# Optimization experiments

Measured on AMD Instinct MI355X. Metric: run time of the kernel, lower is better.

Reference implementation:

```python
import jax, jax.numpy as jnp
import numpy as np

B, S, D_MODEL, D_OUT = 4, 4096, 512, 64


def setup_inputs() -> dict:
    key = jax.random.key(0)
    ks = jax.random.split(key, 10)
    query = jax.random.normal(ks[0], (B, S, D_MODEL), dtype=jnp.float32)
    key_t = jax.random.normal(ks[1], (B, S, D_MODEL), dtype=jnp.float32)
    value = jax.random.normal(ks[2], (B, S, D_MODEL), dtype=jnp.float32)
    mask = jax.random.randint(ks[3], (B, S, S), 0, 2, dtype=jnp.int32)
    sc = 1.0 / np.sqrt(D_MODEL)
    Wq = jax.random.uniform(ks[4], (D_MODEL, D_OUT), minval=-sc, maxval=sc, dtype=jnp.float32)
    bq = jnp.zeros((D_OUT,), dtype=jnp.float32)
    Wk = jax.random.uniform(ks[5], (D_MODEL, D_OUT), minval=-sc, maxval=sc, dtype=jnp.float32)
    bk = jnp.zeros((D_OUT,), dtype=jnp.float32)
    Wv = jax.random.uniform(ks[6], (D_MODEL, D_OUT), minval=-sc, maxval=sc, dtype=jnp.float32)
    bv = jnp.zeros((D_OUT,), dtype=jnp.float32)
    return {"query": query, "key": key_t, "value": value, "mask": mask,
            "Wq": Wq, "bq": bq, "Wk": Wk, "bk": bk, "Wv": Wv, "bv": bv}


def reference(query, key, value, mask, Wq, bq, Wk, bk, Wv, bv):
    # Linear projections (single head): [B,S,D_MODEL] @ [D_MODEL,D_OUT] + bias
    q = jnp.einsum('bsd,de->bse', query, Wq) + bq
    k = jnp.einsum('bsd,de->bse', key, Wk) + bk
    v = jnp.einsum('bsd,de->bse', value, Wv) + bv
    dim_k = k.shape[-1]
    scores = jnp.einsum('bqe,bke->bqk', q, k) / jnp.sqrt(jnp.float32(dim_k))  # [B,S,S]
    scores = jnp.where(mask == 0, -jnp.inf, scores)
    weights = jax.nn.softmax(scores, axis=-1)
    # dropout is identity in eval mode / for deterministic reference
    outputs = jnp.einsum('bqk,bke->bqe', weights, v)  # [B,S,D_OUT]
    return outputs
```

## Files before the change

### kernel.cpp

```cpp
#include <hip/hip_runtime.h>
#include <hip/hip_bf16.h>

#define BB 4
#define SS 4096
#define DMODEL 512
#define DOUT 64
#define NKH 2
#define KH (SS / NKH)
#define NIT (KH / 64)

typedef __bf16 bf16_t;
typedef __bf16 bf16x8 __attribute__((ext_vector_type(8)));
typedef float floatx4 __attribute__((ext_vector_type(4)));

__device__ inline void gl_lds16(const void* g, void* l) {
  __builtin_amdgcn_global_load_lds(
      (const __attribute__((address_space(1))) unsigned int*)g,
      (__attribute__((address_space(3))) unsigned int*)l, 16, 0, 0);
}

__global__ __launch_bounds__(256) void wtrans_kernel(
    const float* __restrict__ Wq, const float* __restrict__ Wk,
    const float* __restrict__ Wv, bf16_t* __restrict__ wT) {
  int idx = blockIdx.x * 256 + threadIdx.x;
  int mat = idx >> 12;
  int r   = idx & 4095;
  int e   = r & 63;
  int d0  = (r >> 6) << 3;
  const float* W = (mat == 0) ? Wq : ((mat == 1) ? Wk : Wv);
  bf16_t* dst = wT + (size_t)mat * (DOUT * DMODEL) + (size_t)e * DMODEL + d0;
#pragma unroll
  for (int j = 0; j < 8; ++j) dst[j] = (bf16_t)W[(size_t)(d0 + j) * DOUT + e];
}

__global__ __launch_bounds__(256) void proj_kernel(
    const float* __restrict__ inq, const float* __restrict__ ink,
    const float* __restrict__ inv, const bf16_t* __restrict__ wT,
    const float* __restrict__ bq, const float* __restrict__ bk,
    const float* __restrict__ bv,
    bf16_t* __restrict__ q_ws, bf16_t* __restrict__ k_ws,
    bf16_t* __restrict__ v_wsT) {
  const int mat = blockIdx.x >> 8;
  const int s0  = (blockIdx.x & 255) << 6;
  const int lane = threadIdx.x & 63;
  const int w    = threadIdx.x >> 6;
  const int col  = lane & 15, quad = lane >> 4;

  const float* inp  = (mat == 0) ? inq : ((mat == 1) ? ink : inv);
  const float* bias = (mat == 0) ? bq : ((mat == 1) ? bk : bv);
  const bf16_t* wt  = wT + (size_t)mat * (DOUT * DMODEL);

  const int arow = s0 + w * 16 + col;
  floatx4 acc[4] = {};

  for (int ch = 0; ch < 16; ++ch) {
    const int d0 = ch * 32 + quad * 8;
    float4 a0 = *(const float4*)(inp + (size_t)arow * DMODEL + d0);
    float4 a1 = *(const float4*)(inp + (size_t)arow * DMODEL + d0 + 4);
    bf16x8 af;
    af[0] = (bf16_t)a0.x; af[1] = (bf16_t)a0.y; af[2] = (bf16_t)a0.z; af[3] = (bf16_t)a0.w;
    af[4] = (bf16_t)a1.x; af[5] = (bf16_t)a1.y; af[6] = (bf16_t)a1.z; af[7] = (bf16_t)a1.w;
#pragma unroll
    for (int c = 0; c < 4; ++c) {
      bf16x8 bw = *(const bf16x8*)(wt + (size_t)(c * 16 + col) * DMODEL + d0);
      acc[c] = __builtin_amdgcn_mfma_f32_16x16x32_bf16(af, bw, acc[c], 0, 0, 0);
    }
  }

#pragma unroll
  for (int c = 0; c < 4; ++c) {
    float bcol = bias[c * 16 + col];
#pragma unroll
    for (int r = 0; r < 4; ++r) {
      int row = s0 + w * 16 + quad * 4 + r;
      float v = acc[c][r] + bcol;
      if (mat == 2) {
        int b = row >> 12, sp = row & 4095;
        v_wsT[((size_t)(b * DOUT + c * 16 + col)) * SS + sp] = (bf16_t)v;
      } else {
        bf16_t* dst = (mat == 0) ? q_ws : k_ws;
        dst[(size_t)row * DOUT + c * 16 + col] = (bf16_t)v;
      }
    }
  }
}

__global__ __launch_bounds__(256, 2) void attn_kernel(
    const bf16_t* __restrict__ q_ws, const bf16_t* __restrict__ k_ws,
    const bf16_t* __restrict__ v_wsT, const int* __restrict__ mask,
    float* __restrict__ O_part, float* __restrict__ l_part) {
  const int bq = blockIdx.x >> 1, kh = blockIdx.x & 1;
  const int b  = bq >> 6;
  const int q0 = (bq & 63) << 6;
  const int kbase = kh * KH;
  const int lane = threadIdx.x & 63;
  const int wi   = threadIdx.x >> 6;
  const int col  = lane & 15, quad = lane >> 4;

  __shared__ __align__(16) bf16_t Kb[2][64 * 64];
  __shared__ __align__(16) bf16_t Vb[2][64 * 64];
  __shared__ __align__(16) bf16_t Pl[4][16][72];

  const int qrowA = q0 + wi * 16 + col;
  const bf16_t* qbase = q_ws + ((size_t)(b * SS) + qrowA) * DOUT + quad * 8;
  const bf16x8 qa0 = *(const bf16x8*)(qbase);
  const bf16x8 qa1 = *(const bf16x8*)(qbase + 32);
  const int* mrow = mask + ((size_t)(b * SS) + qrowA) * SS + quad * 8;

  const int srow = lane >> 3;
  const int schk = (lane & 7) ^ srow;

  auto stage = [&](int it, int buf) {
    const int k0 = kbase + it * 64;
#pragma unroll
    for (int j = 0; j < 2; ++j) {
      const int i = wi * 2 + j;
      const int r = i * 8 + srow;
      const char* gK = (const char*)(k_ws + ((size_t)(b * SS) + k0 + r) * DOUT) + schk * 16;
      gl_lds16(gK, (char*)(&Kb[buf][0]) + i * 1024);
      const char* gV = (const char*)(v_wsT + ((size_t)(b * DOUT) + r) * SS + k0) + schk * 16;
      gl_lds16(gV, (char*)(&Vb[buf][0]) + i * 1024);
    }
  };

  int4 mc[2][2], mn[2][2];
  auto loadM = [&](int k0, int4 m[2][2]) {
#pragma unroll
    for (int s = 0; s < 2; ++s) {
      const int4* mp = (const int4*)(mrow + k0 + s * 32);
      m[s][0] = mp[0];
      m[s][1] = mp[1];
    }
  };

  floatx4 o[4] = {};
  float l_acc = 0.f;
  const bf16_t* prow_r = &Pl[wi][col][quad * 8];

  stage(0, 0);
  loadM(kbase, mc);
  __syncthreads();

  for (int it = 0; it < NIT; ++it) {
    const int buf = it & 1;
    const int itn = (it + 1 < NIT) ? it + 1 : it;

    loadM(kbase + itn * 64, mn);
    stage(itn, buf ^ 1);

    floatx4 sacc[4];
#pragma unroll
    for (int c = 0; c < 4; ++c) {
      const int row = c * 16 + col;
      bf16x8 k0f = *(const bf16x8*)((const char*)&Kb[buf][0] + row * 128 + ((quad ^ (col & 7)) * 16));
      bf16x8 k1f = *(const bf16x8*)((const char*)&Kb[buf][0] + row * 128 + (((4 | quad) ^ (col & 7)) * 16));
      floatx4 z = {};
      z = __builtin_amdgcn_mfma_f32_16x16x32_bf16(qa0, k0f, z, 0, 0, 0);
      z = __builtin_amdgcn_mfma_f32_16x16x32_bf16(qa1, k1f, z, 0, 0, 0);
      sacc[c] = z;
    }

    bf16x8 vc[4][2];
#pragma unroll
    for (int c = 0; c < 4; ++c) {
      const int row = c * 16 + col;
      vc[c][0] = *(const bf16x8*)((const char*)&Vb[buf][0] + row * 128 + ((quad ^ (col & 7)) * 16));
      vc[c][1] = *(const bf16x8*)((const char*)&Vb[buf][0] + row * 128 + (((4 | quad) ^ (col & 7)) * 16));
    }

#pragma unroll
    for (int c = 0; c < 4; ++c)
#pragma unroll
      for (int r = 0; r < 4; ++r)
        Pl[wi][quad * 4 + r][c * 16 + col] = (bf16_t)__expf(sacc[c][r] * 0.125f);

    asm volatile("s_waitcnt lgkmcnt(0)" ::: "memory");

    bf16x8 pa0 = *(const bf16x8*)(prow_r);
    bf16x8 pa1 = *(const bf16x8*)(prow_r + 32);

    float lp = 0.f;
    bf16x8 pm0, pm1;
    auto apply = [&](bf16x8 pa, int4 mlo, int4 mhi, bf16x8& pm) {
      int mm[8] = {mlo.x, mlo.y, mlo.z, mlo.w, mhi.x, mhi.y, mhi.z, mhi.w};
#pragma unroll
      for (int j = 0; j < 8; ++j) {
        bf16_t pv = (mm[j] != 0) ? pa[j] : (bf16_t)0.0f;
        pm[j] = pv;
        lp += (float)pv;
      }
    };
    apply(pa0, mc[0][0], mc[0][1], pm0);
    apply(pa1, mc[1][0], mc[1][1], pm1);
    lp += __shfl_xor(lp, 16);
    lp += __shfl_xor(lp, 32);
    l_acc += lp;

#pragma unroll
    for (int c = 0; c < 4; ++c) {
      o[c] = __builtin_amdgcn_mfma_f32_16x16x32_bf16(pm0, vc[c][0], o[c], 0, 0, 0);
      o[c] = __builtin_amdgcn_mfma_f32_16x16x32_bf16(pm1, vc[c][1], o[c], 0, 0, 0);
    }

    mc[0][0] = mn[0][0]; mc[0][1] = mn[0][1];
    mc[1][0] = mn[1][0]; mc[1][1] = mn[1][1];

    __syncthreads();
  }

  float* Op = O_part + (size_t)blockIdx.x * 64 * 64;
#pragma unroll
  for (int c = 0; c < 4; ++c)
#pragma unroll
    for (int r = 0; r < 4; ++r)
      Op[(wi * 16 + quad * 4 + r) * 64 + c * 16 + col] = o[c][r];
  if (quad == 0) l_part[(size_t)blockIdx.x * 64 + wi * 16 + col] = l_acc;
}

__global__ __launch_bounds__(256) void combine_kernel(
    const float* __restrict__ O_part, const float* __restrict__ l_part,
    float* __restrict__ out) {
  const int idx = blockIdx.x * 256 + threadIdx.x;
  const int base = idx * 4;
  const int row = base >> 6;
  const int c   = base & 63;
  const int t   = row >> 6;
  const int rl  = row & 63;
  const float* p0 = O_part + (((size_t)(t * 2 + 0) * 64 + rl) * 64 + c);
  const float* p1 = O_part + (((size_t)(t * 2 + 1) * 64 + rl) * 64 + c);
  const float inv = 1.0f / (l_part[(size_t)(t * 2) * 64 + rl] +
                            l_part[(size_t)(t * 2 + 1) * 64 + rl]);
  float4 a = *(const float4*)p0;
  float4 b = *(const float4*)p1;
  float4 r4 = {(a.x + b.x) * inv, (a.y + b.y) * inv,
               (a.z + b.z) * inv, (a.w + b.w) * inv};
  *(float4*)(out + base) = r4;
}

extern "C" void kernel_launch(void* const* d_in, const int* in_sizes, int n_in,
                              void* d_out, int out_size, void* d_ws, size_t ws_size,
                              hipStream_t stream) {
  const float* query = (const float*)d_in[0];
  const float* key   = (const float*)d_in[1];
  const float* value = (const float*)d_in[2];
  const int*   mask  = (const int*)d_in[3];
  const float* Wq = (const float*)d_in[4];
  const float* bq = (const float*)d_in[5];
  const float* Wk = (const float*)d_in[6];
  const float* bk = (const float*)d_in[7];
  const float* Wv = (const float*)d_in[8];
  const float* bv = (const float*)d_in[9];
  float* out = (float*)d_out;

  bf16_t* q_ws  = (bf16_t*)d_ws;
  bf16_t* k_ws  = q_ws + (size_t)BB * SS * DOUT;
  bf16_t* v_wsT = k_ws + (size_t)BB * SS * DOUT;
  bf16_t* wT    = v_wsT + (size_t)BB * SS * DOUT;
  float*  O_part = (float*)(wT + 3 * DOUT * DMODEL);
  float*  l_part = O_part + (size_t)512 * 64 * 64;

  hipLaunchKernelGGL(wtrans_kernel, dim3(48), dim3(256), 0, stream, Wq, Wk, Wv, wT);
  hipLaunchKernelGGL(proj_kernel, dim3(768), dim3(256), 0, stream,
                     query, key, value, wT, bq, bk, bv, q_ws, k_ws, v_wsT);
  hipLaunchKernelGGL(attn_kernel, dim3(512), dim3(256), 0, stream,
                     q_ws, k_ws, v_wsT, mask, O_part, l_part);
  hipLaunchKernelGGL(combine_kernel, dim3(1024), dim3(256), 0, stream,
                     O_part, l_part, out);
}
```

Measured before the change: 473.6 us.

## Pre-pack int32 attention mask into bitmask with a separate ballot kernel

Adds a maskpack kernel that streams the int32 mask once and uses wave ballots to compress it into 64-bit bitmasks, one bit per key. The attention kernel then loads one u64 per row per 64-key tile instead of 256 bytes of int32 mask, and selects probabilities with bit tests. The goal is to take the large, latency-heavy mask stream out of the attention inner loop and shrink register pressure there. In exchange it adds an extra kernel launch that still reads the full mask, so total mask traffic is not reduced.

```diff
diff --git a/kernel.cpp b/kernel.cpp
--- a/kernel.cpp
+++ b/kernel.cpp
@@ -12,6 +12,8 @@
 typedef __bf16 bf16_t;
 typedef __bf16 bf16x8 __attribute__((ext_vector_type(8)));
 typedef float floatx4 __attribute__((ext_vector_type(4)));
+typedef unsigned long long u64;
+typedef u64 u64x2 __attribute__((ext_vector_type(2)));
 
 __device__ inline void gl_lds16(const void* g, void* l) {
   __builtin_amdgcn_global_load_lds(
@@ -31,6 +33,25 @@
   bf16_t* dst = wT + (size_t)mat * (DOUT * DMODEL) + (size_t)e * DMODEL + d0;
 #pragma unroll
   for (int j = 0; j < 8; ++j) dst[j] = (bf16_t)W[(size_t)(d0 + j) * DOUT + e];
+}
+
+__global__ __launch_bounds__(256) void maskpack_kernel(
+    const int* __restrict__ mask, u64* __restrict__ bits) {
+  const int wid  = (blockIdx.x * 256 + threadIdx.x) >> 6;
+  const int lane = threadIdx.x & 63;
+  const int* base = mask + (size_t)wid * 1024;
+  u64* wbase = bits + (size_t)wid * 16;
+#pragma unroll
+  for (int c = 0; c < 4; ++c) {
+    const int* p = base + c * 256;
+    u64 b0 = __ballot(p[lane] != 0);
+    u64 b1 = __ballot(p[lane + 64] != 0);
+    u64 b2 = __ballot(p[lane + 128] != 0);
+    u64 b3 = __ballot(p[lane + 192] != 0);
+    u64x2 w01 = {b0, b1}, w23 = {b2, b3};
+    if (lane == 0) *(u64x2*)(wbase + c * 4) = w01;
+    if (lane == 1) *(u64x2*)(wbase + c * 4 + 2) = w23;
+  }
 }
 
 __global__ __launch_bounds__(256) void proj_kernel(
@@ -87,7 +108,7 @@
 
 __global__ __launch_bounds__(256, 2) void attn_kernel(
     const bf16_t* __restrict__ q_ws, const bf16_t* __restrict__ k_ws,
-    const bf16_t* __restrict__ v_wsT, const int* __restrict__ mask,
+    const bf16_t* __restrict__ v_wsT, const u64* __restrict__ bits,
     float* __restrict__ O_part, float* __restrict__ l_part) {
   const int bq = blockIdx.x >> 1, kh = blockIdx.x & 1;
   const int b  = bq >> 6;
@@ -105,7 +126,7 @@
   const bf16_t* qbase = q_ws + ((size_t)(b * SS) + qrowA) * DOUT + quad * 8;
   const bf16x8 qa0 = *(const bf16x8*)(qbase);
   const bf16x8 qa1 = *(const bf16x8*)(qbase + 32);
-  const int* mrow = mask + ((size_t)(b * SS) + qrowA) * SS + quad * 8;
+  const u64* brow = bits + ((size_t)(b * SS) + qrowA) * (SS / 64);
 
   const int srow = lane >> 3;
   const int schk = (lane & 7) ^ srow;
@@ -123,30 +144,20 @@
     }
   };
 
-  int4 mc[2][2], mn[2][2];
-  auto loadM = [&](int k0, int4 m[2][2]) {
-#pragma unroll
-    for (int s = 0; s < 2; ++s) {
-      const int4* mp = (const int4*)(mrow + k0 + s * 32);
-      m[s][0] = mp[0];
-      m[s][1] = mp[1];
-    }
-  };
-
   floatx4 o[4] = {};
   float l_acc = 0.f;
   const bf16_t* prow_r = &Pl[wi][col][quad * 8];
 
   stage(0, 0);
-  loadM(kbase, mc);
+  u64 bits_cur = brow[kbase >> 6];
   __syncthreads();
 
   for (int it = 0; it < NIT; ++it) {
     const int buf = it & 1;
     const int itn = (it + 1 < NIT) ? it + 1 : it;
 
-    loadM(kbase + itn * 64, mn);
     stage(itn, buf ^ 1);
+    u64 bits_nxt = brow[(kbase + itn * 64) >> 6];
 
     floatx4 sacc[4];
 #pragma unroll
@@ -179,19 +190,19 @@
     bf16x8 pa0 = *(const bf16x8*)(prow_r);
     bf16x8 pa1 = *(const bf16x8*)(prow_r + 32);
 
+    unsigned lo32 = (unsigned)bits_cur;
+    unsigned hi32 = (unsigned)(bits_cur >> 32);
+    unsigned m8a = (lo32 >> (quad * 8)) & 0xffu;
+    unsigned m8b = (hi32 >> (quad * 8)) & 0xffu;
     float lp = 0.f;
     bf16x8 pm0, pm1;
-    auto apply = [&](bf16x8 pa, int4 mlo, int4 mhi, bf16x8& pm) {
-      int mm[8] = {mlo.x, mlo.y, mlo.z, mlo.w, mhi.x, mhi.y, mhi.z, mhi.w};
-#pragma unroll
-      for (int j = 0; j < 8; ++j) {
-        bf16_t pv = (mm[j] != 0) ? pa[j] : (bf16_t)0.0f;
-        pm[j] = pv;
-        lp += (float)pv;
-      }
-    };
-    apply(pa0, mc[0][0], mc[0][1], pm0);
-    apply(pa1, mc[1][0], mc[1][1], pm1);
+#pragma unroll
+    for (int j = 0; j < 8; ++j) {
+      bf16_t p0 = ((m8a >> j) & 1u) ? pa0[j] : (bf16_t)0.0f;
+      bf16_t p1 = ((m8b >> j) & 1u) ? pa1[j] : (bf16_t)0.0f;
+      pm0[j] = p0; pm1[j] = p1;
+      lp += (float)p0 + (float)p1;
+    }
     lp += __shfl_xor(lp, 16);
     lp += __shfl_xor(lp, 32);
     l_acc += lp;
@@ -202,9 +213,7 @@
       o[c] = __builtin_amdgcn_mfma_f32_16x16x32_bf16(pm1, vc[c][1], o[c], 0, 0, 0);
     }
 
-    mc[0][0] = mn[0][0]; mc[0][1] = mn[0][1];
-    mc[1][0] = mn[1][0]; mc[1][1] = mn[1][1];
-
+    bits_cur = bits_nxt;
     __syncthreads();
   }
 
@@ -258,12 +267,15 @@
   bf16_t* wT    = v_wsT + (size_t)BB * SS * DOUT;
   float*  O_part = (float*)(wT + 3 * DOUT * DMODEL);
   float*  l_part = O_part + (size_t)512 * 64 * 64;
-
+  u64*    bits   = (u64*)(l_part + 512 * 64);
+
+  hipLaunchKernelGGL(maskpack_kernel, dim3(BB * SS * SS / 1024 / 4), dim3(256), 0, stream,
+                     mask, bits);
   hipLaunchKernelGGL(wtrans_kernel, dim3(48), dim3(256), 0, stream, Wq, Wk, Wv, wT);
   hipLaunchKernelGGL(proj_kernel, dim3(768), dim3(256), 0, stream,
                      query, key, value, wT, bq, bk, bv, q_ws, k_ws, v_wsT);
   hipLaunchKernelGGL(attn_kernel, dim3(512), dim3(256), 0, stream,
-                     q_ws, k_ws, v_wsT, mask, O_part, l_part);
+                     q_ws, k_ws, v_wsT, bits, O_part, l_part);
   hipLaunchKernelGGL(combine_kernel, dim3(1024), dim3(256), 0, stream,
                      O_part, l_part, out);
 }
```

Result: slower. 499.8 us (+5.5%).
